# Optimization experiments

Hardware: AMD Instinct MI355X
Metric: run time of the kernel (lower is better)

## Reference

```python
import jax, jax.numpy as jnp
import numpy as np

VOCAB = 32000
MAX_LEN = 40
DIM_HIDDEN = 1024
DIM_WORD = 512
DIM_VID = 4096
BOS_ID = 0


def lstm_step(x, h, c, w_ih, w_hh, b_ih, b_hh):
    # torch LSTM gate order: i, f, g, o
    gates = x @ w_ih.T + b_ih + h @ w_hh.T + b_hh  # (1, 4H)
    i, f, g, o = jnp.split(gates, 4, axis=-1)
    c_new = jax.nn.sigmoid(f) * c + jax.nn.sigmoid(i) * jnp.tanh(g)
    h_new = jax.nn.sigmoid(o) * jnp.tanh(c_new)
    return h_new, c_new


def setup_inputs() -> dict:
    key = jax.random.key(0)
    ks = jax.random.split(key, 12)
    s1 = 1.0 / np.sqrt(DIM_HIDDEN)
    H = DIM_HIDDEN
    return {
        "vid_feats": jax.random.normal(ks[0], (1, DIM_VID), jnp.float32),
        "w_ih1": jax.random.uniform(ks[1], (4 * H, DIM_VID), jnp.float32, -s1, s1),
        "w_hh1": jax.random.uniform(ks[2], (4 * H, H), jnp.float32, -s1, s1),
        "b_ih1": jax.random.uniform(ks[3], (4 * H,), jnp.float32, -s1, s1),
        "b_hh1": jax.random.uniform(ks[4], (4 * H,), jnp.float32, -s1, s1),
        "w_ih2": jax.random.uniform(ks[5], (4 * H, H + DIM_WORD), jnp.float32, -s1, s1),
        "w_hh2": jax.random.uniform(ks[6], (4 * H, H), jnp.float32, -s1, s1),
        "b_ih2": jax.random.uniform(ks[7], (4 * H,), jnp.float32, -s1, s1),
        "b_hh2": jax.random.uniform(ks[8], (4 * H,), jnp.float32, -s1, s1),
        "emb": jax.random.normal(ks[9], (VOCAB, DIM_WORD), jnp.float32),
        "w_out": jax.random.uniform(ks[10], (VOCAB, H), jnp.float32, -s1, s1),
        "b_out": jax.random.uniform(ks[11], (VOCAB,), jnp.float32, -s1, s1),
    }


def reference(vid_feats, w_ih1, w_hh1, b_ih1, b_hh1, w_ih2, w_hh2, b_ih2, b_hh2, emb, w_out, b_out):
    H = DIM_HIDDEN
    zeros_h = jnp.zeros((1, H), vid_feats.dtype)
    pad_vid = jnp.zeros((1, DIM_VID), vid_feats.dtype)
    pad_word = jnp.zeros((1, DIM_WORD), vid_feats.dtype)

    # encode phase: one step of each LSTM (vid feats + padding word)
    h1, c1 = lstm_step(vid_feats, zeros_h, zeros_h, w_ih1, w_hh1, b_ih1, b_hh1)
    inp2 = jnp.concatenate([h1, pad_word], axis=1)
    h2, c2 = lstm_step(inp2, zeros_h, zeros_h, w_ih2, w_hh2, b_ih2, b_hh2)
    idx0 = jnp.int32(BOS_ID)  # output2 is overwritten with bos_id in the source

    def step(carry, _):
        h1, c1, h2, c2, idx = carry
        h1, c1 = lstm_step(pad_vid, h1, c1, w_ih1, w_hh1, b_ih1, b_hh1)
        embedded = emb[idx].reshape(1, -1)  # (1, dim_word)
        inp2 = jnp.concatenate([h1, embedded], axis=1)
        h2, c2 = lstm_step(inp2, h2, c2, w_ih2, w_hh2, b_ih2, b_hh2)
        logits = h2 @ w_out.T + b_out  # (1, vocab)
        logp = jax.nn.log_softmax(logits, axis=-1)
        # faithful to source: topk over the HIDDEN output, not logits
        idx = jnp.argmax(h2[0]).astype(jnp.int32)
        return (h1, c1, h2, c2, idx), logp

    _, prob_sentence = jax.lax.scan(step, (h1, c1, h2, c2, idx0), None, length=MAX_LEN - 1)
    return prob_sentence  # (max_len-1, 1, vocab)
```

## Files before the change

### kernel.cpp

```cpp
#include <hip/hip_runtime.h>
#include <hip/hip_fp16.h>

typedef unsigned u32x4 __attribute__((ext_vector_type(4)));

#define HID    1024
#define DVID   4096
#define DWORD  512
#define XLEN   (HID + DWORD)
#define NVOCAB 32000
#define NSTEP  39
#define NT     256
#define NWPB   (NT / 64)
#define TT     8
#define NPASS  ((NSTEP + TT - 1) / TT)
#define NEG_BIG (-3.402823466e38f)
#define MAGIC_VAL 0x5EEDF11Du

#define CTRL_BYTES 65536
#define RBAR_W   0
#define H2F_W    1024
#define FBAR_W   2048
#define G1_OFF   65536
#define G2A_OFF  (G1_OFF  + 32768)
#define G2B_OFF  (G2A_OFF + 32768)
#define H2B_OFF  (G2B_OFF + 32768)
#define PM_OFF   (H2B_OFF + 159744)
#define PS_OFF   (PM_OFF  + 159744)
#define MAGIC_OFF (PS_OFF + 159744)
#define W16_OFF  (MAGIC_OFF + 256)
#define W16_BYTES ((size_t)NVOCAB * HID * 2)
#define WIH2_OFF (W16_OFF + W16_BYTES)
#define WIH2_BYTES ((size_t)DVID * XLEN * 2)
#define WHH1_OFF (WIH2_OFF + WIH2_BYTES)
#define WHH_BYTES ((size_t)DVID * HID * 2)
#define WHH2_OFF (WHH1_OFF + WHH_BYTES)
#define WS_T1 ((size_t)W16_OFF + W16_BYTES)
#define WS_T2 ((size_t)WHH2_OFF + WHH_BYTES)

#define FENCE_REL() __builtin_amdgcn_fence(__ATOMIC_RELEASE, "agent")
#define FENCE_ACQ() __builtin_amdgcn_fence(__ATOMIC_ACQUIRE, "agent")

__device__ __forceinline__ float gload(float* p) {
    return __hip_atomic_load(p, __ATOMIC_RELAXED, __HIP_MEMORY_SCOPE_AGENT);
}
__device__ __forceinline__ void gstore(float* p, float v) {
    __hip_atomic_store(p, v, __ATOMIC_RELAXED, __HIP_MEMORY_SCOPE_AGENT);
}
__device__ __forceinline__ unsigned gloadu(unsigned* p) {
    return __hip_atomic_load(p, __ATOMIC_RELAXED, __HIP_MEMORY_SCOPE_AGENT);
}
__device__ __forceinline__ void gstoreu(unsigned* p, unsigned v) {
    __hip_atomic_store(p, v, __ATOMIC_RELAXED, __HIP_MEMORY_SCOPE_AGENT);
}

__device__ __forceinline__ float fast_sigmoid(float x) { return 1.f / (1.f + __expf(-x)); }
__device__ __forceinline__ float fast_tanh(float x)    { return 1.f - 2.f / (__expf(2.f * x) + 1.f); }

__device__ __forceinline__ float wave_reduce(float v) {
#pragma unroll
    for (int o = 32; o; o >>= 1) v += __shfl_xor(v, o, 64);
    return v;
}
__device__ __forceinline__ int wave_reduce_i(int v) {
// ... 11 lines not shown
    if (v > m) { s = s * __expf(m - v) + 1.f; m = v; } else s += __expf(v - m);
}

template<int LEN>
__device__ __forceinline__ float row_dotT(const float* __restrict__ w, const float* x, int lane) {
    float a = 0.f;
#pragma unroll
    for (int q = lane * 4; q < LEN; q += 256) {
        float4 wv = *(const float4*)(w + q);
        float4 xv = *(const float4*)(x + q);
        a = fmaf(wv.x, xv.x, a); a = fmaf(wv.y, xv.y, a);
        a = fmaf(wv.z, xv.z, a); a = fmaf(wv.w, xv.w, a);
    }
    return wave_reduce(a);
}
__device__ __forceinline__ void row_dot2(const float* __restrict__ wa, const float* xa,
                                         const float* __restrict__ wb, const float* xb,
                                         int lane, float& ra, float& rb) {
    float a = 0.f, b = 0.f;
#pragma unroll
    for (int q = lane * 4; q < HID; q += 256) {
        float4 w1 = *(const float4*)(wa + q);
        float4 w2 = *(const float4*)(wb + q);
        float4 x1 = *(const float4*)(xa + q);
        float4 x2 = *(const float4*)(xb + q);
        a = fmaf(w1.x, x1.x, a); a = fmaf(w1.y, x1.y, a);
        a = fmaf(w1.z, x1.z, a); a = fmaf(w1.w, x1.w, a);
        b = fmaf(w2.x, x2.x, b); b = fmaf(w2.y, x2.y, b);
        b = fmaf(w2.z, x2.z, b); b = fmaf(w2.w, x2.w, b);
    }
    ra = wave_reduce(a); rb = wave_reduce(b);
}

__device__ __forceinline__ float hlo(unsigned u) {
    return __half2float(__ushort_as_half((unsigned short)(u & 0xffffu)));
}
__device__ __forceinline__ float hhi(unsigned u) {
    return __half2float(__ushort_as_half((unsigned short)(u >> 16)));
}
__device__ __forceinline__ u32x4 ntld(const unsigned short* p) {
    return __builtin_nontemporal_load((const u32x4*)p);
}

template<int LEN>
__device__ __forceinline__ float row_dotT_h(const unsigned short* __restrict__ w, const float* x, int lane) {
    float a = 0.f;
#pragma unroll
    for (int q = lane * 8; q < LEN; q += 512) {
        u32x4 u = *(const u32x4*)(w + q);
        float4 x0 = *(const float4*)(x + q);
        float4 x1 = *(const float4*)(x + q + 4);
        a = fmaf(hlo(u.x), x0.x, a); a = fmaf(hhi(u.x), x0.y, a);
        a = fmaf(hlo(u.y), x0.z, a); a = fmaf(hhi(u.y), x0.w, a);
        a = fmaf(hlo(u.z), x1.x, a); a = fmaf(hhi(u.z), x1.y, a);
        a = fmaf(hlo(u.w), x1.z, a); a = fmaf(hhi(u.w), x1.w, a);
    }
    return wave_reduce(a);
}
__device__ __forceinline__ void row_dot2_h(const unsigned short* __restrict__ wa, const float* xa,
                                           const unsigned short* __restrict__ wb, const float* xb,
                                           int lane, float& ra, float& rb) {
    float a = 0.f, b = 0.f;
#pragma unroll
    for (int q = lane * 8; q < HID; q += 512) {
        u32x4 ua = *(const u32x4*)(wa + q);
        u32x4 ub = *(const u32x4*)(wb + q);
        float4 xa0 = *(const float4*)(xa + q);
        float4 xa1 = *(const float4*)(xa + q + 4);
        float4 xb0 = *(const float4*)(xb + q);
        float4 xb1 = *(const float4*)(xb + q + 4);
        a = fmaf(hlo(ua.x), xa0.x, a); a = fmaf(hhi(ua.x), xa0.y, a);
        a = fmaf(hlo(ua.y), xa0.z, a); a = fmaf(hhi(ua.y), xa0.w, a);
        a = fmaf(hlo(ua.z), xa1.x, a); a = fmaf(hhi(ua.z), xa1.y, a);
        a = fmaf(hlo(ua.w), xa1.z, a); a = fmaf(hhi(ua.w), xa1.w, a);
        b = fmaf(hlo(ub.x), xb0.x, b); b = fmaf(hhi(ub.x), xb0.y, b);
        b = fmaf(hlo(ub.y), xb0.z, b); b = fmaf(hhi(ub.y), xb0.w, b);
        b = fmaf(hlo(ub.z), xb1.x, b); b = fmaf(hhi(ub.z), xb1.y, b);
        b = fmaf(hlo(ub.w), xb1.z, b); b = fmaf(hhi(ub.w), xb1.w, b);
    }
    ra = wave_reduce(a); rb = wave_reduce(b);
}

#define DOT16H(acc, u0, u1)                                                \
    acc = fmaf(hlo(u0.x), x0.x, acc); acc = fmaf(hhi(u0.x), x0.y, acc);    \
    acc = fmaf(hlo(u0.y), x0.z, acc); acc = fmaf(hhi(u0.y), x0.w, acc);    \
    acc = fmaf(hlo(u0.z), x1.x, acc); acc = fmaf(hhi(u0.z), x1.y, acc);    \
    acc = fmaf(hlo(u0.w), x1.z, acc); acc = fmaf(hhi(u0.w), x1.w, acc);    \
    acc = fmaf(hlo(u1.x), x2.x, acc); acc = fmaf(hhi(u1.x), x2.y, acc);    \
    acc = fmaf(hlo(u1.y), x2.z, acc); acc = fmaf(hhi(u1.y), x2.w, acc);    \
    acc = fmaf(hlo(u1.z), x3.x, acc); acc = fmaf(hhi(u1.z), x3.y, acc);    \
    acc = fmaf(hlo(u1.w), x3.z, acc); acc = fmaf(hhi(u1.w), x3.w, acc);

__device__ __forceinline__ void lstm_update1(float* G, float* c, float* h, int tid) {
#pragma unroll
    for (int j = tid; j < HID; j += NT) {
        float gi = gload(G + j), gf = gload(G + j + HID);
        float gg = gload(G + j + 2 * HID), go = gload(G + j + 3 * HID);
        float cn = fast_sigmoid(gf) * c[j] + fast_sigmoid(gi) * fast_tanh(gg);
        c[j] = cn;
        h[j] = fast_sigmoid(go) * fast_tanh(cn);
    }
}
__device__ __forceinline__ void lstm_update2(float* Ga, float* Gb, float* c, float* h, int tid) {
#pragma unroll
    for (int j = tid; j < HID; j += NT) {
        float gi = gload(Ga + j) + gload(Gb + j);
        float gf = gload(Ga + j + HID) + gload(Gb + j + HID);
        float gg = gload(Ga + j + 2 * HID) + gload(Gb + j + 2 * HID);
        float go = gload(Ga + j + 3 * HID) + gload(Gb + j + 3 * HID);
        float cn = fast_sigmoid(gf) * c[j] + fast_sigmoid(gi) * fast_tanh(gg);
        c[j] = cn;
        h[j] = fast_sigmoid(go) * fast_tanh(cn);
    }
}

__device__ __forceinline__ void gbar(unsigned* base, int line, unsigned target, int tid, int lane) {
    __syncthreads();
    if (tid < 64) {
        if (lane == 0)
            __hip_atomic_fetch_add(base + line * 32, 1u, __ATOMIC_RELAXED, __HIP_MEMORY_SCOPE_AGENT);
        for (;;) {
            unsigned v = (lane < 16) ? gloadu(base + lane * 32) : 0u;
            if ((unsigned)wave_reduce_i((int)v) >= target) break;
            __builtin_amdgcn_s_sleep(4);
        }
    }
    __syncthreads();
}
// ... 18 lines not shown
        r.y = __half_as_ushort(__float2half(v.y));
        r.z = __half_as_ushort(__float2half(v.z));
        r.w = __half_as_ushort(__float2half(v.w));
        *(ushort4*)(d + off) = r;
    }
}

__global__ __launch_bounds__(NT, 4) void seq2seq_kernel(
    const float* __restrict__ vid,
    const float* __restrict__ w_ih1, const float* __restrict__ w_hh1,
    const float* __restrict__ b_ih1, const float* __restrict__ b_hh1,
    const float* __restrict__ w_ih2, const float* __restrict__ w_hh2,
    const float* __restrict__ b_ih2, const float* __restrict__ b_hh2,
    const float* __restrict__ emb,  const float* __restrict__ w_out,
    const float* __restrict__ b_out,
    int use16, int useh, int nr, int nl,
    float* __restrict__ out, char* wsb, unsigned* magicp)
{
    const int tid  = threadIdx.x;
    const int lane = tid & 63;
    const int wib  = tid >> 6;
    const int bid  = blockIdx.x;
    const int nb   = nr + nl;

    unsigned* ctrl = (unsigned*)wsb;
    unsigned* rbar = ctrl + RBAR_W;
    unsigned* h2f  = ctrl + H2F_W;
    unsigned* fbar = ctrl + FBAR_W;
    float* G1g = (float*)(wsb + G1_OFF);
    float* G2a = (float*)(wsb + G2A_OFF);
    float* G2b = (float*)(wsb + G2B_OFF);
    float* h2b = (float*)(wsb + H2B_OFF);
    float* PM  = (float*)(wsb + PM_OFF);
    float* PS  = (float*)(wsb + PS_OFF);
    const unsigned short* w16   = (const unsigned short*)(wsb + W16_OFF);
    const unsigned short* wih2h = (const unsigned short*)(wsb + WIH2_OFF);
    const unsigned short* whh1h = (const unsigned short*)(wsb + WHH1_OFF);
    const unsigned short* whh2h = (const unsigned short*)(wsb + WHH2_OFF);

    __shared__ __align__(16) float sMem[TT * HID];
    float* sX  = sMem;
    float* sC1 = sMem + XLEN;
    float* sC2 = sMem + XLEN + HID;
    float* sH2 = sMem + XLEN + 2 * HID;
    float* sXT = sMem;
    __shared__ float sRm[NWPB], sRs[NWPB];
    __shared__ int   sRi[NWPB];
    __shared__ int   sIdx;
    __shared__ float sPm[NWPB][TT], sPs[NWPB][TT];
    __shared__ float sOff[NSTEP];

    if (magicp && bid == 0 && tid == 0) gstoreu(magicp, MAGIC_VAL);

    const bool isrec = (bid < nr);
    const int  lb    = bid - nr;
    const int  chunk = (NVOCAB + nl - 1) / nl;
    const int  begin = isrec ? 0 : lb * chunk;
    const int  end   = isrec ? 0 : min(begin + chunk, NVOCAB);
    const bool active = (!isrec) && (begin < end);
    unsigned tgt = 0;

    for (int j = tid; j < HID; j += NT) { sC1[j] = 0.f; sC2[j] = 0.f; }
    if (tid == 0) sIdx = 0;
    __syncthreads();
    {
        const int nwr = nb * NWPB, gw = bid * NWPB + wib;
        {
            int ch = (4096 + nwr - 1) / nwr;
            int b0 = gw * ch, e0 = min(b0 + ch, 4096);
            for (int r = b0; r < e0; ++r) {
                float v = row_dotT<DVID>(w_ih1 + (size_t)r * DVID, vid, lane);
                if (lane == 0) gstore(&G1g[4096 + r], v + b_ih1[r] + b_hh1[r]);
            }
        }
        tgt += nb; gbar(rbar, bid & 15, tgt, tid, lane);
        lstm_update1(G1g + 4096, sC1, sX, tid);
        for (int j = tid; j < DWORD; j += NT) sX[HID + j] = 0.f;
        __syncthreads();
        {
            int ch = (8192 + nwr - 1) / nwr;
            int b0 = gw * ch, e0 = min(b0 + ch, 8192);
            for (int task = b0; task < e0; ++task) {
                if (task < 4096) {
                    int r = task;
                    float v = row_dotT<XLEN>(w_ih2 + (size_t)r * XLEN, sX, lane);
                    if (lane == 0) gstore(&G2a[4096 + r], v + b_ih2[r] + b_hh2[r]);
                } else {
                    int r = task - 4096;
                    float v = row_dotT<HID>(w_hh1 + (size_t)r * HID, sX, lane);
                    if (lane == 0) { gstore(&G1g[r], v + b_ih1[r] + b_hh1[r]); gstore(&G2b[4096 + r], 0.f); }
                }
            }
        }
        tgt += nb; gbar(rbar, bid & 15, tgt, tid, lane);
    }

    if (isrec) {
        __builtin_amdgcn_s_setprio(2);
        const int nwr = nr * NWPB, gw = bid * NWPB + wib;
        lstm_update2(G2a + 4096, G2b + 4096, sC2, sH2, tid);
        __syncthreads();

        for (int t = 0; t < NSTEP; ++t) {
            const int cb = (t & 1) * 4096, nb2 = ((t + 1) & 1) * 4096;
            lstm_update1(G1g + cb, sC1, sX, tid);
            {
                const float* erow = emb + (size_t)sIdx * DWORD;
                for (int j = tid; j < DWORD; j += NT) sX[HID + j] = erow[j];
            }
            __syncthreads();
            {
                int ch = (8192 + nwr - 1) / nwr;
                int b0 = gw * ch, e0 = min(b0 + ch, 8192);
                if (useh) {
                    for (int task = b0; task < e0; ++task) {
                        if (task < 4096) {
                            int r = task;
                            float v = row_dotT_h<XLEN>(wih2h + (size_t)r * XLEN, sX, lane);
                            if (lane == 0) gstore(&G2a[cb + r], v + b_ih2[r] + b_hh2[r]);
                        } else {
                            int r = task - 4096;
                            float va, vb;
                            row_dot2_h(whh2h + (size_t)r * HID, sH2,
                                       whh1h + (size_t)r * HID, sX, lane, va, vb);
                            if (lane == 0) {
                                gstore(&G2b[cb + r], va);
                                if (t < NSTEP - 1) gstore(&G1g[nb2 + r], vb + b_ih1[r] + b_hh1[r]);
                            }
                        }
                    }
                } else {
                    for (int task = b0; task < e0; ++task) {
                        if (task < 4096) {
                            int r = task;
                            float v = row_dotT<XLEN>(w_ih2 + (size_t)r * XLEN, sX, lane);
                            if (lane == 0) gstore(&G2a[cb + r], v + b_ih2[r] + b_hh2[r]);
                        } else {
                            int r = task - 4096;
                            float va, vb;
                            row_dot2(w_hh2 + (size_t)r * HID, sH2,
                                     w_hh1 + (size_t)r * HID, sX, lane, va, vb);
                            if (lane == 0) {
                                gstore(&G2b[cb + r], va);
                                if (t < NSTEP - 1) gstore(&G1g[nb2 + r], vb + b_ih1[r] + b_hh1[r]);
                            }
                        }
                    }
                }
            }
            tgt += nr; gbar(rbar, bid & 15, tgt, tid, lane);

            lstm_update2(G2a + cb, G2b + cb, sC2, sH2, tid);
            __syncthreads();
            if (bid == 0)
                for (int j = tid; j < HID; j += NT) gstore(&h2b[(size_t)t * HID + j], sH2[j]);
            {
                float bm = NEG_BIG; int bi = 0;
                for (int j = tid; j < HID; j += NT) {
                    float v = sH2[j];
                    if (v > bm) { bm = v; bi = j; }
                }
#pragma unroll
                for (int o = 32; o; o >>= 1) {
                    float vm = __shfl_xor(bm, o, 64); int vi = __shfl_xor(bi, o, 64);
                    if (vm > bm || (vm == bm && vi < bi)) { bm = vm; bi = vi; }
                }
                if (lane == 0) { sRm[wib] = bm; sRi[wib] = bi; }
                __syncthreads();
                if (tid == 0) {
                    float m0 = sRm[0]; int i0 = sRi[0];
                    for (int w = 1; w < NWPB; ++w)
                        if (sRm[w] > m0 || (sRm[w] == m0 && sRi[w] < i0)) { m0 = sRm[w]; i0 = sRi[w]; }
                    sIdx = i0;
                }
            }
            __syncthreads();
            if (bid == 0 && tid == 0) {
#pragma unroll
                for (int i = 0; i < 8; ++i)
                    gstoreu(h2f + i * 32, (unsigned)(t + 1));
            }
        }
    } else if (active) {
        unsigned* myflag = h2f + (lb & 7) * 32;

        if (use16) {
            unsigned acc = 0u;
            for (int r = begin + wib; r < end; r += NWPB) {
                u32x4 a = ntld(w16 + (size_t)r * HID + lane * 8);
                u32x4 b2 = ntld(w16 + (size_t)r * HID + 512 + lane * 8);
                acc += a.x + b2.x;
            }
            asm volatile("" :: "v"(acc));
        }

        for (int pass = 0; pass < NPASS; ++pass) {
            const int t0 = pass * TT;
            const int tn = (NSTEP - t0 < TT) ? (NSTEP - t0) : TT;
            const unsigned twait = (unsigned)(t0 + tn);
            if (tid == 0) {
                while (gloadu(myflag) < twait) __builtin_amdgcn_s_sleep(16);
            }
            __syncthreads();
            for (int i = tid; i < tn * HID; i += NT)
                sXT[i] = gload(&h2b[(size_t)t0 * HID + i]);
            __syncthreads();

            float m[TT], s[TT];
#pragma unroll
            for (int k = 0; k < TT; ++k) { m[k] = NEG_BIG; s[k] = 0.f; }

            if (use16) {
                const int qe = begin + ((end - begin) & ~3);
                for (int r = begin + wib * 4; r < qe; r += NWPB * 4) {
                    const unsigned short* wp = w16 + (size_t)r * HID + lane * 8;
                    u32x4 ua0 = ntld(wp);            u32x4 ua1 = ntld(wp + 512);
                    u32x4 ub0 = ntld(wp + HID);      u32x4 ub1 = ntld(wp + HID + 512);
                    u32x4 uc0 = ntld(wp + 2 * HID);  u32x4 uc1 = ntld(wp + 2 * HID + 512);
                    u32x4 ud0 = ntld(wp + 3 * HID);  u32x4 ud1 = ntld(wp + 3 * HID + 512);
                    float b0v = b_out[r], b1v = b_out[r + 1], b2v = b_out[r + 2], b3v = b_out[r + 3];
#pragma unroll
                    for (int k = 0; k < TT; ++k) {
                        if (t0 + k < NSTEP) {
                            const float* xp = sXT + k * HID + lane * 8;
                            float4 x0 = *(const float4*)(xp);
                            float4 x1 = *(const float4*)(xp + 4);
                            float4 x2 = *(const float4*)(xp + 512);
                            float4 x3 = *(const float4*)(xp + 516);
                            float a0 = 0.f, a1 = 0.f, a2 = 0.f, a3 = 0.f;
                            DOT16H(a0, ua0, ua1)
                            DOT16H(a1, ub0, ub1)
                            DOT16H(a2, uc0, uc1)
                            DOT16H(a3, ud0, ud1)
                            float v0 = wave_reduce(a0) + b0v;
                            float v1 = wave_reduce(a1) + b1v;
                            float v2 = wave_reduce(a2) + b2v;
                            float v3 = wave_reduce(a3) + b3v;
                            if (lane == 0) {
                                float* op = out + (size_t)(t0 + k) * NVOCAB + r;
                                op[0] = v0; op[1] = v1; op[2] = v2; op[3] = v3;
                            }
                            online_upd(m[k], s[k], v0); online_upd(m[k], s[k], v1);
                            online_upd(m[k], s[k], v2); online_upd(m[k], s[k], v3);
                        }
                    }
                }
                for (int r = qe + wib; r < end; r += NWPB) {
                    const unsigned short* wp = w16 + (size_t)r * HID + lane * 8;
                    u32x4 u0 = ntld(wp);
                    u32x4 u1 = ntld(wp + 512);
                    float bv = b_out[r];
#pragma unroll
                    for (int k = 0; k < TT; ++k) {
                        if (t0 + k < NSTEP) {
                            const float* xp = sXT + k * HID + lane * 8;
                            float4 x0 = *(const float4*)(xp);
                            float4 x1 = *(const float4*)(xp + 4);
                            float4 x2 = *(const float4*)(xp + 512);
                            float4 x3 = *(const float4*)(xp + 516);
                            float a = 0.f;
                            DOT16H(a, u0, u1)
                            float v = wave_reduce(a) + bv;
                            if (lane == 0) out[(size_t)(t0 + k) * NVOCAB + r] = v;
                            online_upd(m[k], s[k], v);
                        }
                    }
                }
            } else {
                for (int r = begin + wib; r < end; r += NWPB) {
                    const float* wp = w_out + (size_t)r * HID;
                    float bv = b_out[r];
#pragma unroll
                    for (int k = 0; k < TT; ++k) {
                        if (t0 + k < NSTEP) {
                            float v = row_dotT<HID>(wp, sXT + k * HID, lane) + bv;
                            if (lane == 0) out[(size_t)(t0 + k) * NVOCAB + r] = v;
                            online_upd(m[k], s[k], v);
                        }
                    }
                }
            }

            if (lane == 0) {
#pragma unroll
                for (int k = 0; k < TT; ++k) { sPm[wib][k] = m[k]; sPs[wib][k] = s[k]; }
            }
            __syncthreads();
            if (tid == 0) {
#pragma unroll
                for (int k = 0; k < TT; ++k) {
// ... 58 lines not shown
    const float* b_ih1 = (const float*)d_in[3];
    const float* b_hh1 = (const float*)d_in[4];
    const float* w_ih2 = (const float*)d_in[5];
    const float* w_hh2 = (const float*)d_in[6];
    const float* b_ih2 = (const float*)d_in[7];
    const float* b_hh2 = (const float*)d_in[8];
    const float* emb   = (const float*)d_in[9];
    const float* w_out = (const float*)d_in[10];
    const float* b_out = (const float*)d_in[11];
    float* out = (float*)d_out;
    char* wsb  = (char*)d_ws;

    int use16 = (ws_size >= WS_T1) ? 1 : 0;
    int useh  = (ws_size >= WS_T2) ? 1 : 0;
    unsigned* magicp = (ws_size >= (size_t)MAGIC_OFF + 256) ? (unsigned*)(wsb + MAGIC_OFF) : (unsigned*)0;

    hipMemsetAsync(d_ws, 0, CTRL_BYTES, stream);

    if (use16 && magicp) {
        int n0 = NVOCAB * HID;
        int n1 = useh ? DVID * XLEN : 0;
        int n2 = useh ? DVID * HID : 0;
        int n3 = useh ? DVID * HID : 0;
        cvt_all<<<dim3(2048), dim3(256), 0, stream>>>(
            w_out, w_ih2, w_hh1, w_hh2,
            (unsigned short*)(wsb + W16_OFF), (unsigned short*)(wsb + WIH2_OFF),
            (unsigned short*)(wsb + WHH1_OFF), (unsigned short*)(wsb + WHH2_OFF),
            n0, n1, n2, n3, magicp);
    } else {
        use16 = 0; useh = 0;
    }

    int occ = 0;
    if (hipOccupancyMaxActiveBlocksPerMultiprocessor(&occ, seq2seq_kernel, NT, 0) != hipSuccess || occ < 1)
        occ = 1;
    int nb = occ * 256;
    if (nb > 1024) nb = 1024;
    nb &= ~3;
    if (nb < 4) nb = 4;
    int nr = nb >> 2, nl = nb - nr;

    void* args[] = { &vid, &w_ih1, &w_hh1, &b_ih1, &b_hh1,
                     &w_ih2, &w_hh2, &b_ih2, &b_hh2,
                     &emb, &w_out, &b_out, &use16, &useh, &nr, &nl, &out, &wsb, &magicp };
    hipLaunchCooperativeKernel((const void*)seq2seq_kernel,
                               dim3(nb), dim3(NT), args, 0, stream);
}
```

Before: 1.665 ms.

## Partition LSTM recurrence into 64 unit-owning blocks with packed fp16 dot2 math

Restructures the recurrent phase so a fixed set of 64 blocks each own a slice of hidden units. Each block computes all four gates for its units locally and exchanges only h vectors through global buffers, instead of the whole gate vector being reduced and redistributed. It also switches the fp16 weight dot products to packed fdot2 with fp16-packed activations, and restructures the vocab projection to reuse each weight load across 8 time steps. The argmax is now done through per-block partials. This adds an extra grid barrier in the encode phase, changes the block split, and adds fp16 rounding of activations.

```diff
diff --git a/kernel.cpp b/kernel.cpp
--- a/kernel.cpp
+++ b/kernel.cpp
@@ -2,6 +2,8 @@
 #include <hip/hip_fp16.h>
 
 typedef unsigned u32x4 __attribute__((ext_vector_type(4)));
+typedef unsigned u32x2 __attribute__((ext_vector_type(2)));
+typedef _Float16 h2v  __attribute__((ext_vector_type(2)));
 
 #define HID    1024
 #define DVID   4096
@@ -11,42 +13,47 @@
 #define NSTEP  39
 #define NT     256
 #define NWPB   (NT / 64)
+#define NR     64
+#define U      (HID / NR)
 #define TT     8
 #define NPASS  ((NSTEP + TT - 1) / TT)
 #define NEG_BIG (-3.402823466e38f)
-#define MAGIC_VAL 0x5EEDF11Du
+#define MAGIC_VAL 0x5EEDF22Du
 
 #define CTRL_BYTES 65536
 #define RBAR_W   0
 #define H2F_W    1024
 #define FBAR_W   2048
-#define G1_OFF   65536
-#define G2A_OFF  (G1_OFF  + 32768)
-#define G2B_OFF  (G2A_OFF + 32768)
-#define H2B_OFF  (G2B_OFF + 32768)
-#define PM_OFF   (H2B_OFF + 159744)
-#define PS_OFF   (PM_OFF  + 159744)
-#define MAGIC_OFF (PS_OFF + 159744)
-#define W16_OFF  (MAGIC_OFF + 256)
-#define W16_BYTES ((size_t)NVOCAB * HID * 2)
-#define WIH2_OFF (W16_OFF + W16_BYTES)
+#define GE_OFF    65536
+#define GE2_OFF   (GE_OFF  + 16384)
+#define H1B_OFF   (GE2_OFF + 16384)
+#define H2BF_OFF  (H1B_OFF + 8192)
+#define PV_OFF    (H2BF_OFF + 8192)
+#define PI_OFF    (PV_OFF  + 512)
+#define H2B_OFF   (PI_OFF  + 512)
+#define PM_OFF    (H2B_OFF + 159744)
+#define PS_OFF    (PM_OFF  + 159744)
+#define MAGIC_OFF (PS_OFF  + 159744)
+#define W16_OFF   (MAGIC_OFF + 256)
+#define W16_BYTES  ((size_t)NVOCAB * HID * 2)
+#define WIH2_OFF  (W16_OFF + W16_BYTES)
 #define WIH2_BYTES ((size_t)DVID * XLEN * 2)
-#define WHH1_OFF (WIH2_OFF + WIH2_BYTES)
-#define WHH_BYTES ((size_t)DVID * HID * 2)
-#define WHH2_OFF (WHH1_OFF + WHH_BYTES)
-#define WS_T1 ((size_t)W16_OFF + W16_BYTES)
-#define WS_T2 ((size_t)WHH2_OFF + WHH_BYTES)
+#define WHH1_OFF  (WIH2_OFF + WIH2_BYTES)
+#define WHH_BYTES  ((size_t)DVID * HID * 2)
+#define WHH2_OFF  (WHH1_OFF + WHH_BYTES)
+#define WS_T1  ((size_t)W16_OFF + W16_BYTES)
+#define WS_T2  ((size_t)WHH2_OFF + WHH_BYTES)
 
 #define FENCE_REL() __builtin_amdgcn_fence(__ATOMIC_RELEASE, "agent")
 #define FENCE_ACQ() __builtin_amdgcn_fence(__ATOMIC_ACQUIRE, "agent")
 
-__device__ __forceinline__ float gload(float* p) {
-    return __hip_atomic_load(p, __ATOMIC_RELAXED, __HIP_MEMORY_SCOPE_AGENT);
+__device__ __forceinline__ float gload(const float* p) {
+    return __hip_atomic_load((const float*)p, __ATOMIC_RELAXED, __HIP_MEMORY_SCOPE_AGENT);
 }
 __device__ __forceinline__ void gstore(float* p, float v) {
     __hip_atomic_store(p, v, __ATOMIC_RELAXED, __HIP_MEMORY_SCOPE_AGENT);
 }
-__device__ __forceinline__ unsigned gloadu(unsigned* p) {
+__device__ __forceinline__ unsigned gloadu(const unsigned* p) {
     return __hip_atomic_load(p, __ATOMIC_RELAXED, __HIP_MEMORY_SCOPE_AGENT);
 }
 __device__ __forceinline__ void gstoreu(unsigned* p, unsigned v) {
@@ -88,104 +95,20 @@
     }
     return wave_reduce(a);
 }
-__device__ __forceinline__ void row_dot2(const float* __restrict__ wa, const float* xa,
-                                         const float* __restrict__ wb, const float* xb,
-                                         int lane, float& ra, float& rb) {
-    float a = 0.f, b = 0.f;
-#pragma unroll
-    for (int q = lane * 4; q < HID; q += 256) {
-        float4 w1 = *(const float4*)(wa + q);
-        float4 w2 = *(const float4*)(wb + q);
-        float4 x1 = *(const float4*)(xa + q);
-        float4 x2 = *(const float4*)(xb + q);
-        a = fmaf(w1.x, x1.x, a); a = fmaf(w1.y, x1.y, a);
-        a = fmaf(w1.z, x1.z, a); a = fmaf(w1.w, x1.w, a);
-        b = fmaf(w2.x, x2.x, b); b = fmaf(w2.y, x2.y, b);
-        b = fmaf(w2.z, x2.z, b); b = fmaf(w2.w, x2.w, b);
-    }
-    ra = wave_reduce(a); rb = wave_reduce(b);
-}
-
-__device__ __forceinline__ float hlo(unsigned u) {
-    return __half2float(__ushort_as_half((unsigned short)(u & 0xffffu)));
-}
-__device__ __forceinline__ float hhi(unsigned u) {
-    return __half2float(__ushort_as_half((unsigned short)(u >> 16)));
-}
-__device__ __forceinline__ u32x4 ntld(const unsigned short* p) {
+
+__device__ __forceinline__ float fd2(unsigned w, unsigned x, float a) {
+    return __builtin_amdgcn_fdot2(__builtin_bit_cast(h2v, w), __builtin_bit_cast(h2v, x), a, false);
+}
+__device__ __forceinline__ unsigned pk2(float a, float b) {
+    unsigned short lo = __half_as_ushort(__float2half(a));
+    unsigned short hi = __half_as_ushort(__float2half(b));
+    return (unsigned)lo | ((unsigned)hi << 16);
+}
+__device__ __forceinline__ u32x4 ntld4(const unsigned* p) {
     return __builtin_nontemporal_load((const u32x4*)p);
 }
-
-template<int LEN>
-__device__ __forceinline__ float row_dotT_h(const unsigned short* __restrict__ w, const float* x, int lane) {
-    float a = 0.f;
-#pragma unroll
-    for (int q = lane * 8; q < LEN; q += 512) {
-        u32x4 u = *(const u32x4*)(w + q);
-        float4 x0 = *(const float4*)(x + q);
-        float4 x1 = *(const float4*)(x + q + 4);
-        a = fmaf(hlo(u.x), x0.x, a); a = fmaf(hhi(u.x), x0.y, a);
-        a = fmaf(hlo(u.y), x0.z, a); a = fmaf(hhi(u.y), x0.w, a);
-        a = fmaf(hlo(u.z), x1.x, a); a = fmaf(hhi(u.z), x1.y, a);
-        a = fmaf(hlo(u.w), x1.z, a); a = fmaf(hhi(u.w), x1.w, a);
-    }
-    return wave_reduce(a);
-}
-__device__ __forceinline__ void row_dot2_h(const unsigned short* __restrict__ wa, const float* xa,
-                                           const unsigned short* __restrict__ wb, const float* xb,
-                                           int lane, float& ra, float& rb) {
-    float a = 0.f, b = 0.f;
-#pragma unroll
-    for (int q = lane * 8; q < HID; q += 512) {
-        u32x4 ua = *(const u32x4*)(wa + q);
-        u32x4 ub = *(const u32x4*)(wb + q);
-        float4 xa0 = *(const float4*)(xa + q);
-        float4 xa1 = *(const float4*)(xa + q + 4);
-        float4 xb0 = *(const float4*)(xb + q);
-        float4 xb1 = *(const float4*)(xb + q + 4);
-        a = fmaf(hlo(ua.x), xa0.x, a); a = fmaf(hhi(ua.x), xa0.y, a);
-        a = fmaf(hlo(ua.y), xa0.z, a); a = fmaf(hhi(ua.y), xa0.w, a);
-        a = fmaf(hlo(ua.z), xa1.x, a); a = fmaf(hhi(ua.z), xa1.y, a);
-        a = fmaf(hlo(ua.w), xa1.z, a); a = fmaf(hhi(ua.w), xa1.w, a);
-        b = fmaf(hlo(ub.x), xb0.x, b); b = fmaf(hhi(ub.x), xb0.y, b);
-        b = fmaf(hlo(ub.y), xb0.z, b); b = fmaf(hhi(ub.y), xb0.w, b);
-        b = fmaf(hlo(ub.z), xb1.x, b); b = fmaf(hhi(ub.z), xb1.y, b);
-        b = fmaf(hlo(ub.w), xb1.z, b); b = fmaf(hhi(ub.w), xb1.w, b);
-    }
-    ra = wave_reduce(a); rb = wave_reduce(b);
-}
-
-#define DOT16H(acc, u0, u1)                                                \
-    acc = fmaf(hlo(u0.x), x0.x, acc); acc = fmaf(hhi(u0.x), x0.y, acc);    \
-    acc = fmaf(hlo(u0.y), x0.z, acc); acc = fmaf(hhi(u0.y), x0.w, acc);    \
-    acc = fmaf(hlo(u0.z), x1.x, acc); acc = fmaf(hhi(u0.z), x1.y, acc);    \
-    acc = fmaf(hlo(u0.w), x1.z, acc); acc = fmaf(hhi(u0.w), x1.w, acc);    \
-    acc = fmaf(hlo(u1.x), x2.x, acc); acc = fmaf(hhi(u1.x), x2.y, acc);    \
-    acc = fmaf(hlo(u1.y), x2.z, acc); acc = fmaf(hhi(u1.y), x2.w, acc);    \
-    acc = fmaf(hlo(u1.z), x3.x, acc); acc = fmaf(hhi(u1.z), x3.y, acc);    \
-    acc = fmaf(hlo(u1.w), x3.z, acc); acc = fmaf(hhi(u1.w), x3.w, acc);
-
-__device__ __forceinline__ void lstm_update1(float* G, float* c, float* h, int tid) {
-#pragma unroll
-    for (int j = tid; j < HID; j += NT) {
-        float gi = gload(G + j), gf = gload(G + j + HID);
-        float gg = gload(G + j + 2 * HID), go = gload(G + j + 3 * HID);
-        float cn = fast_sigmoid(gf) * c[j] + fast_sigmoid(gi) * fast_tanh(gg);
-        c[j] = cn;
-        h[j] = fast_sigmoid(go) * fast_tanh(cn);
-    }
-}
-__device__ __forceinline__ void lstm_update2(float* Ga, float* Gb, float* c, float* h, int tid) {
-#pragma unroll
-    for (int j = tid; j < HID; j += NT) {
-        float gi = gload(Ga + j) + gload(Gb + j);
-        float gf = gload(Ga + j + HID) + gload(Gb + j + HID);
-        float gg = gload(Ga + j + 2 * HID) + gload(Gb + j + 2 * HID);
-        float go = gload(Ga + j + 3 * HID) + gload(Gb + j + 3 * HID);
-        float cn = fast_sigmoid(gf) * c[j] + fast_sigmoid(gi) * fast_tanh(gg);
-        c[j] = cn;
-        h[j] = fast_sigmoid(go) * fast_tanh(cn);
-    }
+__device__ __forceinline__ u32x2 ntld2(const unsigned* p) {
+    return __builtin_nontemporal_load((const u32x2*)p);
 }
 
 __device__ __forceinline__ void gbar(unsigned* base, int line, unsigned target, int tid, int lane) {
@@ -234,55 +157,49 @@
     const float* __restrict__ b_ih2, const float* __restrict__ b_hh2,
     const float* __restrict__ emb,  const float* __restrict__ w_out,
     const float* __restrict__ b_out,
-    int use16, int useh, int nr, int nl,
+    int use16, int useh, int nl,
     float* __restrict__ out, char* wsb, unsigned* magicp)
 {
     const int tid  = threadIdx.x;
     const int lane = tid & 63;
     const int wib  = tid >> 6;
     const int bid  = blockIdx.x;
-    const int nb   = nr + nl;
+    const int nb   = NR + nl;
 
     unsigned* ctrl = (unsigned*)wsb;
     unsigned* rbar = ctrl + RBAR_W;
     unsigned* h2f  = ctrl + H2F_W;
     unsigned* fbar = ctrl + FBAR_W;
-    float* G1g = (float*)(wsb + G1_OFF);
-    float* G2a = (float*)(wsb + G2A_OFF);
-    float* G2b = (float*)(wsb + G2B_OFF);
-    float* h2b = (float*)(wsb + H2B_OFF);
-    float* PM  = (float*)(wsb + PM_OFF);
-    float* PS  = (float*)(wsb + PS_OFF);
-    const unsigned short* w16   = (const unsigned short*)(wsb + W16_OFF);
-    const unsigned short* wih2h = (const unsigned short*)(wsb + WIH2_OFF);
-    const unsigned short* whh1h = (const unsigned short*)(wsb + WHH1_OFF);
-    const unsigned short* whh2h = (const unsigned short*)(wsb + WHH2_OFF);
-
-    __shared__ __align__(16) float sMem[TT * HID];
-    float* sX  = sMem;
-    float* sC1 = sMem + XLEN;
-    float* sC2 = sMem + XLEN + HID;
-    float* sH2 = sMem + XLEN + 2 * HID;
-    float* sXT = sMem;
-    __shared__ float sRm[NWPB], sRs[NWPB];
-    __shared__ int   sRi[NWPB];
-    __shared__ int   sIdx;
+    float* GE    = (float*)(wsb + GE_OFF);
+    float* GE2   = (float*)(wsb + GE2_OFF);
+    float* h1buf = (float*)(wsb + H1B_OFF);
+    float* h2buf = (float*)(wsb + H2BF_OFF);
+    float* PV    = (float*)(wsb + PV_OFF);
+    unsigned* PI = (unsigned*)(wsb + PI_OFF);
+    float* h2b   = (float*)(wsb + H2B_OFF);
+    float* PM    = (float*)(wsb + PM_OFF);
+    float* PS    = (float*)(wsb + PS_OFF);
+    const unsigned* w16u  = (const unsigned*)(wsb + W16_OFF);
+    const unsigned* wih2u = (const unsigned*)(wsb + WIH2_OFF);
+    const unsigned* whh1u = (const unsigned*)(wsb + WHH1_OFF);
+    const unsigned* whh2u = (const unsigned*)(wsb + WHH2_OFF);
+
+    __shared__ __align__(16) unsigned sBuf[4096];
+    __shared__ float sG2[64], sG1[64], sB2v[64], sB1v[64];
+    __shared__ float sC1a[U], sC2a[U], sHo[U];
     __shared__ float sPm[NWPB][TT], sPs[NWPB][TT];
     __shared__ float sOff[NSTEP];
 
     if (magicp && bid == 0 && tid == 0) gstoreu(magicp, MAGIC_VAL);
 
-    const bool isrec = (bid < nr);
-    const int  lb    = bid - nr;
+    const bool isrec = (bid < NR);
+    const int  lb    = bid - NR;
     const int  chunk = (NVOCAB + nl - 1) / nl;
     const int  begin = isrec ? 0 : lb * chunk;
     const int  end   = isrec ? 0 : min(begin + chunk, NVOCAB);
     const bool active = (!isrec) && (begin < end);
     unsigned tgt = 0;
 
-    for (int j = tid; j < HID; j += NT) { sC1[j] = 0.f; sC2[j] = 0.f; }
-    if (tid == 0) sIdx = 0;
-    __syncthreads();
     {
         const int nwr = nb * NWPB, gw = bid * NWPB + wib;
         {
@@ -290,12 +207,25 @@
             int b0 = gw * ch, e0 = min(b0 + ch, 4096);
             for (int r = b0; r < e0; ++r) {
                 float v = row_dotT<DVID>(w_ih1 + (size_t)r * DVID, vid, lane);
-                if (lane == 0) gstore(&G1g[4096 + r], v + b_ih1[r] + b_hh1[r]);
+                if (lane == 0) gstore(GE + r, v + b_ih1[r] + b_hh1[r]);
             }
         }
         tgt += nb; gbar(rbar, bid & 15, tgt, tid, lane);
-        lstm_update1(G1g + 4096, sC1, sX, tid);
-        for (int j = tid; j < DWORD; j += NT) sX[HID + j] = 0.f;
+        if (isrec && tid < U) {
+            int gu = bid * U + tid;
+            float gi = gload(GE + gu), gg = gload(GE + 2048 + gu), go = gload(GE + 3072 + gu);
+            float c1 = fast_sigmoid(gi) * fast_tanh(gg);
+            sC1a[tid] = c1;
+            gstore(h1buf + HID + gu, fast_sigmoid(go) * fast_tanh(c1));
+        }
+        tgt += nb; gbar(rbar, bid & 15, tgt, tid, lane);
+        float* sXf = (float*)sBuf;
+        for (int i = tid * 4; i < HID; i += NT * 4) {
+            float4 v;
+            v.x = gload(h1buf + HID + i);     v.y = gload(h1buf + HID + i + 1);
+            v.z = gload(h1buf + HID + i + 2); v.w = gload(h1buf + HID + i + 3);
+            *(float4*)(sXf + i) = v;
+        }
         __syncthreads();
         {
             int ch = (8192 + nwr - 1) / nwr;
@@ -303,12 +233,12 @@
             for (int task = b0; task < e0; ++task) {
                 if (task < 4096) {
                     int r = task;
-                    float v = row_dotT<XLEN>(w_ih2 + (size_t)r * XLEN, sX, lane);
-                    if (lane == 0) gstore(&G2a[4096 + r], v + b_ih2[r] + b_hh2[r]);
+                    float v = row_dotT<HID>(w_ih2 + (size_t)r * XLEN, sXf, lane);
+                    if (lane == 0) gstore(GE2 + r, v + b_ih2[r] + b_hh2[r]);
                 } else {
                     int r = task - 4096;
-                    float v = row_dotT<HID>(w_hh1 + (size_t)r * HID, sX, lane);
-                    if (lane == 0) { gstore(&G1g[r], v + b_ih1[r] + b_hh1[r]); gstore(&G2b[4096 + r], 0.f); }
+                    float v = row_dotT<HID>(w_hh1 + (size_t)r * HID, sXf, lane);
+                    if (lane == 0) gstore(GE + r, v + b_ih1[r] + b_hh1[r]);
                 }
             }
         }
@@ -317,98 +247,199 @@
 
     if (isrec) {
         __builtin_amdgcn_s_setprio(2);
-        const int nwr = nr * NWPB, gw = bid * NWPB + wib;
-        lstm_update2(G2a + 4096, G2b + 4096, sC2, sH2, tid);
-        __syncthreads();
+        if (tid < U) {
+            int gu = bid * U + tid;
+            float gi = gload(GE2 + gu), gg = gload(GE2 + 2048 + gu), go = gload(GE2 + 3072 + gu);
+            float c2 = fast_sigmoid(gi) * fast_tanh(gg);
+            sC2a[tid] = c2;
+            gstore(h2buf + HID + gu, fast_sigmoid(go) * fast_tanh(c2));
+            gi = gload(GE + gu); float gf = gload(GE + 1024 + gu);
+            gg = gload(GE + 2048 + gu); go = gload(GE + 3072 + gu);
+            float c1 = fast_sigmoid(gf) * sC1a[tid] + fast_sigmoid(gi) * fast_tanh(gg);
+            sC1a[tid] = c1;
+            gstore(h1buf + gu, fast_sigmoid(go) * fast_tanh(c1));
+        }
+        if (tid < 64) {
+            int rr = (tid & 3) * HID + bid * U + (tid >> 2);
+            sB2v[tid] = b_ih2[rr] + b_hh2[rr];
+            sB1v[tid] = b_ih1[rr] + b_hh1[rr];
+        }
+        tgt += NR; gbar(rbar, bid & 15, tgt, tid, lane);
+
+        unsigned* sXh  = sBuf;
+        unsigned* sH2h = sBuf + 768;
+        float*    sXf32 = (float*)sBuf;
+
+        const int g  = lane >> 2, gl = lane & 3;
+        const int d  = wib * 16 + g;
+        const int r2 = (d & 3) * HID + bid * U + (d >> 2);
 
         for (int t = 0; t < NSTEP; ++t) {
-            const int cb = (t & 1) * 4096, nb2 = ((t + 1) & 1) * 4096;
-            lstm_update1(G1g + cb, sC1, sX, tid);
-            {
-                const float* erow = emb + (size_t)sIdx * DWORD;
-                for (int j = tid; j < DWORD; j += NT) sX[HID + j] = erow[j];
+            if (wib == 0) {
+                unsigned idx = 0;
+                if (t > 0) {
+                    const int par = (t + 1) & 1;
+                    float av = gload(PV + par * NR + lane);
+                    unsigned ai = gloadu(PI + par * NR + lane);
+#pragma unroll
+                    for (int o = 32; o; o >>= 1) {
+                        float vm = __shfl_xor(av, o, 64);
+                        unsigned im = (unsigned)__shfl_xor((int)ai, o, 64);
+                        if (vm > av || (vm == av && im < ai)) { av = vm; ai = im; }
+                    }
+                    idx = ai;
+                }
+                const float* er = emb + (size_t)idx * DWORD + lane * 8;
+                float4 e0 = *(const float4*)(er), e1 = *(const float4*)(er + 4);
+                if (useh) {
+                    u32x4 p;
+                    p.x = pk2(e0.x, e0.y); p.y = pk2(e0.z, e0.w);
+                    p.z = pk2(e1.x, e1.y); p.w = pk2(e1.z, e1.w);
+                    *(u32x4*)(sXh + 512 + lane * 4) = p;
+                } else {
+                    *(float4*)(sXf32 + HID + lane * 8) = e0;
+                    *(float4*)(sXf32 + HID + lane * 8 + 4) = e1;
+                }
+            } else if (wib < 3) {
+                int j = tid - 64;
+                const float* hp = h1buf + (t & 1) * HID + j * 8;
+                float v[8];
+#pragma unroll
+                for (int e2 = 0; e2 < 8; ++e2) v[e2] = gload(hp + e2);
+                if (useh) {
+                    u32x4 p;
+                    p.x = pk2(v[0], v[1]); p.y = pk2(v[2], v[3]);
+                    p.z = pk2(v[4], v[5]); p.w = pk2(v[6], v[7]);
+                    *(u32x4*)(sXh + j * 4) = p;
+                } else {
+                    float4 a = {v[0], v[1], v[2], v[3]}, b = {v[4], v[5], v[6], v[7]};
+                    *(float4*)(sXf32 + j * 8) = a;
+                    *(float4*)(sXf32 + j * 8 + 4) = b;
+                }
+            } else {
+                int j = tid - 192;
+                const float* hp = h2buf + ((t + 1) & 1) * HID + j * 16;
+                float v[16];
+#pragma unroll
+                for (int e2 = 0; e2 < 16; ++e2) v[e2] = gload(hp + e2);
+                if (useh) {
+                    u32x4 p0, p1;
+                    p0.x = pk2(v[0], v[1]);  p0.y = pk2(v[2], v[3]);
+                    p0.z = pk2(v[4], v[5]);  p0.w = pk2(v[6], v[7]);
+                    p1.x = pk2(v[8], v[9]);  p1.y = pk2(v[10], v[11]);
+                    p1.z = pk2(v[12], v[13]); p1.w = pk2(v[14], v[15]);
+                    *(u32x4*)(sH2h + j * 8) = p0;
+                    *(u32x4*)(sH2h + j * 8 + 4) = p1;
+                } else {
+                    *(float4*)(sXf32 + 1536 + j * 16)      = {v[0], v[1], v[2], v[3]};
+                    *(float4*)(sXf32 + 1536 + j * 16 + 4)  = {v[4], v[5], v[6], v[7]};
+                    *(float4*)(sXf32 + 1536 + j * 16 + 8)  = {v[8], v[9], v[10], v[11]};
+                    *(float4*)(sXf32 + 1536 + j * 16 + 12) = {v[12], v[13], v[14], v[15]};
+                }
             }
             __syncthreads();
-            {
-                int ch = (8192 + nwr - 1) / nwr;
-                int b0 = gw * ch, e0 = min(b0 + ch, 8192);
-                if (useh) {
-                    for (int task = b0; task < e0; ++task) {
-                        if (task < 4096) {
-                            int r = task;
-                            float v = row_dotT_h<XLEN>(wih2h + (size_t)r * XLEN, sX, lane);
-                            if (lane == 0) gstore(&G2a[cb + r], v + b_ih2[r] + b_hh2[r]);
-                        } else {
-                            int r = task - 4096;
-                            float va, vb;
-                            row_dot2_h(whh2h + (size_t)r * HID, sH2,
-                                       whh1h + (size_t)r * HID, sX, lane, va, vb);
-                            if (lane == 0) {
-                                gstore(&G2b[cb + r], va);
-                                if (t < NSTEP - 1) gstore(&G1g[nb2 + r], vb + b_ih1[r] + b_hh1[r]);
-                            }
-                        }
-                    }
-                } else {
-                    for (int task = b0; task < e0; ++task) {
-                        if (task < 4096) {
-                            int r = task;
-                            float v = row_dotT<XLEN>(w_ih2 + (size_t)r * XLEN, sX, lane);
-                            if (lane == 0) gstore(&G2a[cb + r], v + b_ih2[r] + b_hh2[r]);
-                        } else {
-                            int r = task - 4096;
-                            float va, vb;
-                            row_dot2(w_hh2 + (size_t)r * HID, sH2,
-                                     w_hh1 + (size_t)r * HID, sX, lane, va, vb);
-                            if (lane == 0) {
-                                gstore(&G2b[cb + r], va);
-                                if (t < NSTEP - 1) gstore(&G1g[nb2 + r], vb + b_ih1[r] + b_hh1[r]);
-                            }
-                        }
-                    }
-                }
-            }
-            tgt += nr; gbar(rbar, bid & 15, tgt, tid, lane);
-
-            lstm_update2(G2a + cb, G2b + cb, sC2, sH2, tid);
+
+            float a2 = 0.f, a1 = 0.f;
+            if (useh) {
+                const unsigned* wr = wih2u + (size_t)r2 * 768;
+#pragma unroll
+                for (int j = 0; j < 48; ++j) {
+                    u32x4 w = *(const u32x4*)(wr + gl * 4 + j * 16);
+                    u32x4 x = *(const u32x4*)(sXh + gl * 4 + j * 16);
+                    a2 = fd2(w.x, x.x, a2); a2 = fd2(w.y, x.y, a2);
+                    a2 = fd2(w.z, x.z, a2); a2 = fd2(w.w, x.w, a2);
+                }
+                const unsigned* wr2 = whh2u + (size_t)r2 * 512;
+#pragma unroll
+                for (int j = 0; j < 32; ++j) {
+                    u32x4 w = *(const u32x4*)(wr2 + gl * 4 + j * 16);
+                    u32x4 x = *(const u32x4*)(sH2h + gl * 4 + j * 16);
+                    a2 = fd2(w.x, x.x, a2); a2 = fd2(w.y, x.y, a2);
+                    a2 = fd2(w.z, x.z, a2); a2 = fd2(w.w, x.w, a2);
+                }
+                if (t < NSTEP - 1) {
+                    const unsigned* wr1 = whh1u + (size_t)r2 * 512;
+#pragma unroll
+                    for (int j = 0; j < 32; ++j) {
+                        u32x4 w = *(const u32x4*)(wr1 + gl * 4 + j * 16);
+                        u32x4 x = *(const u32x4*)(sXh + gl * 4 + j * 16);
+                        a1 = fd2(w.x, x.x, a1); a1 = fd2(w.y, x.y, a1);
+                        a1 = fd2(w.z, x.z, a1); a1 = fd2(w.w, x.w, a1);
+                    }
+                }
+            } else {
+                const float* wr = w_ih2 + (size_t)r2 * XLEN;
+#pragma unroll 8
+                for (int j = 0; j < 96; ++j) {
+                    float4 w = *(const float4*)(wr + gl * 4 + j * 16);
+                    float4 x = *(const float4*)(sXf32 + gl * 4 + j * 16);
+                    a2 = fmaf(w.x, x.x, a2); a2 = fmaf(w.y, x.y, a2);
+                    a2 = fmaf(w.z, x.z, a2); a2 = fmaf(w.w, x.w, a2);
+                }
+                const float* wr2 = w_hh2 + (size_t)r2 * HID;
+#pragma unroll 8
+                for (int j = 0; j < 64; ++j) {
+                    float4 w = *(const float4*)(wr2 + gl * 4 + j * 16);
+                    float4 x = *(const float4*)(sXf32 + 1536 + gl * 4 + j * 16);
+                    a2 = fmaf(w.x, x.x, a2); a2 = fmaf(w.y, x.y, a2);
+                    a2 = fmaf(w.z, x.z, a2); a2 = fmaf(w.w, x.w, a2);
+                }
+                if (t < NSTEP - 1) {
+                    const float* wr1 = w_hh1 + (size_t)r2 * HID;
+#pragma unroll 8
+                    for (int j = 0; j < 64; ++j) {
+                        float4 w = *(const float4*)(wr1 + gl * 4 + j * 16);
+                        float4 x = *(const float4*)(sXf32 + gl * 4 + j * 16);
+                        a1 = fmaf(w.x, x.x, a1); a1 = fmaf(w.y, x.y, a1);
+                        a1 = fmaf(w.z, x.z, a1); a1 = fmaf(w.w, x.w, a1);
+                    }
+                }
+            }
+            a2 += __shfl_xor(a2, 1, 64); a2 += __shfl_xor(a2, 2, 64);
+            a1 += __shfl_xor(a1, 1, 64); a1 += __shfl_xor(a1, 2, 64);
+            if (gl == 0) { sG2[d] = a2 + sB2v[d]; sG1[d] = a1 + sB1v[d]; }
             __syncthreads();
-            if (bid == 0)
-                for (int j = tid; j < HID; j += NT) gstore(&h2b[(size_t)t * HID + j], sH2[j]);
-            {
-                float bm = NEG_BIG; int bi = 0;
-                for (int j = tid; j < HID; j += NT) {
-                    float v = sH2[j];
-                    if (v > bm) { bm = v; bi = j; }
-                }
-#pragma unroll
-                for (int o = 32; o; o >>= 1) {
-                    float vm = __shfl_xor(bm, o, 64); int vi = __shfl_xor(bi, o, 64);
-                    if (vm > bm || (vm == bm && vi < bi)) { bm = vm; bi = vi; }
-                }
-                if (lane == 0) { sRm[wib] = bm; sRi[wib] = bi; }
-                __syncthreads();
-                if (tid == 0) {
-                    float m0 = sRm[0]; int i0 = sRi[0];
-                    for (int w = 1; w < NWPB; ++w)
-                        if (sRm[w] > m0 || (sRm[w] == m0 && sRi[w] < i0)) { m0 = sRm[w]; i0 = sRi[w]; }
-                    sIdx = i0;
+
+            if (tid < U) {
+                int gu = bid * U + tid;
+                float gi = sG2[tid * 4], gf = sG2[tid * 4 + 1];
+                float gg = sG2[tid * 4 + 2], go = sG2[tid * 4 + 3];
+                float c2 = fast_sigmoid(gf) * sC2a[tid] + fast_sigmoid(gi) * fast_tanh(gg);
+                sC2a[tid] = c2;
+                float hv = fast_sigmoid(go) * fast_tanh(c2);
+                gstore(h2buf + (t & 1) * HID + gu, hv);
+                gstore(h2b + (size_t)t * HID + gu, hv);
+                sHo[tid] = hv;
+                if (t < NSTEP - 1) {
+                    gi = sG1[tid * 4]; gf = sG1[tid * 4 + 1];
+                    gg = sG1[tid * 4 + 2]; go = sG1[tid * 4 + 3];
+                    float c1 = fast_sigmoid(gf) * sC1a[tid] + fast_sigmoid(gi) * fast_tanh(gg);
+                    sC1a[tid] = c1;
+                    gstore(h1buf + ((t + 1) & 1) * HID + gu, fast_sigmoid(go) * fast_tanh(c1));
                 }
             }
             __syncthreads();
+            if (tid == 0) {
+                float bm = sHo[0]; int bi = 0;
+                for (int uu = 1; uu < U; ++uu) if (sHo[uu] > bm) { bm = sHo[uu]; bi = uu; }
+                gstore(PV + (t & 1) * NR + bid, bm);
+                gstoreu(PI + (t & 1) * NR + bid, (unsigned)(bid * U + bi));
+            }
+            tgt += NR; gbar(rbar, bid & 15, tgt, tid, lane);
             if (bid == 0 && tid == 0) {
 #pragma unroll
-                for (int i = 0; i < 8; ++i)
-                    gstoreu(h2f + i * 32, (unsigned)(t + 1));
+                for (int i = 0; i < 8; ++i) gstoreu(h2f + i * 32, (unsigned)(t + 1));
             }
         }
     } else if (active) {
         unsigned* myflag = h2f + (lb & 7) * 32;
+        unsigned* sXT2 = sBuf;
 
         if (use16) {
             unsigned acc = 0u;
             for (int r = begin + wib; r < end; r += NWPB) {
-                u32x4 a = ntld(w16 + (size_t)r * HID + lane * 8);
-                u32x4 b2 = ntld(w16 + (size_t)r * HID + 512 + lane * 8);
+                u32x4 a = ntld4(w16u + (size_t)r * 512 + lane * 8);
+                u32x4 b2 = ntld4(w16u + (size_t)r * 512 + lane * 8 + 4);
                 acc += a.x + b2.x;
             }
             asm volatile("" :: "v"(acc));
@@ -417,13 +448,15 @@
         for (int pass = 0; pass < NPASS; ++pass) {
             const int t0 = pass * TT;
             const int tn = (NSTEP - t0 < TT) ? (NSTEP - t0) : TT;
-            const unsigned twait = (unsigned)(t0 + tn);
             if (tid == 0) {
-                while (gloadu(myflag) < twait) __builtin_amdgcn_s_sleep(16);
+                while (gloadu(myflag) < (unsigned)(t0 + tn)) __builtin_amdgcn_s_sleep(32);
             }
             __syncthreads();
-            for (int i = tid; i < tn * HID; i += NT)
-                sXT[i] = gload(&h2b[(size_t)t0 * HID + i]);
+            for (int wdx = tid; wdx < tn * 512; wdx += NT) {
+                float f0 = gload(h2b + (size_t)t0 * HID + wdx * 2);
+                float f1 = gload(h2b + (size_t)t0 * HID + wdx * 2 + 1);
+                sXT2[wdx] = pk2(f0, f1);
+            }
             __syncthreads();
 
             float m[TT], s[TT];
@@ -431,56 +464,61 @@
             for (int k = 0; k < TT; ++k) { m[k] = NEG_BIG; s[k] = 0.f; }
 
             if (use16) {
-                const int qe = begin + ((end - begin) & ~3);
-                for (int r = begin + wib * 4; r < qe; r += NWPB * 4) {
-                    const unsigned short* wp = w16 + (size_t)r * HID + lane * 8;
-                    u32x4 ua0 = ntld(wp);            u32x4 ua1 = ntld(wp + 512);
-                    u32x4 ub0 = ntld(wp + HID);      u32x4 ub1 = ntld(wp + HID + 512);
-                    u32x4 uc0 = ntld(wp + 2 * HID);  u32x4 uc1 = ntld(wp + 2 * HID + 512);
-                    u32x4 ud0 = ntld(wp + 3 * HID);  u32x4 ud1 = ntld(wp + 3 * HID + 512);
-                    float b0v = b_out[r], b1v = b_out[r + 1], b2v = b_out[r + 2], b3v = b_out[r + 3];
+                int r = begin + wib * 4;
+                for (; r + 3 < end; r += NWPB * 4) {
+                    float acc[4][TT];
+#pragma unroll
+                    for (int j = 0; j < 4; ++j)
+#pragma unroll
+                        for (int k = 0; k < TT; ++k) acc[j][k] = 0.f;
+#pragma unroll
+                    for (int it = 0; it < 4; ++it) {
+                        const int ci = it * 128 + lane * 2;
+                        u32x2 w0 = ntld2(w16u + (size_t)r * 512 + ci);
+                        u32x2 w1 = ntld2(w16u + (size_t)(r + 1) * 512 + ci);
+                        u32x2 w2 = ntld2(w16u + (size_t)(r + 2) * 512 + ci);
+                        u32x2 w3 = ntld2(w16u + (size_t)(r + 3) * 512 + ci);
+#pragma unroll
+                        for (int k = 0; k < TT; ++k) {
+                            u32x2 x = *(const u32x2*)(sXT2 + k * 512 + ci);
+                            acc[0][k] = fd2(w0.x, x.x, acc[0][k]); acc[0][k] = fd2(w0.y, x.y, acc[0][k]);
+                            acc[1][k] = fd2(w1.x, x.x, acc[1][k]); acc[1][k] = fd2(w1.y, x.y, acc[1][k]);
+                            acc[2][k] = fd2(w2.x, x.x, acc[2][k]); acc[2][k] = fd2(w2.y, x.y, acc[2][k]);
+                            acc[3][k] = fd2(w3.x, x.x, acc[3][k]); acc[3][k] = fd2(w3.y, x.y, acc[3][k]);
+                        }
+                    }
+#pragma unroll
+                    for (int j = 0; j < 4; ++j) {
+                        float bv = b_out[r + j];
+#pragma unroll
+                        for (int k = 0; k < TT; ++k) {
+                            if (t0 + k < NSTEP) {
+                                float v = wave_reduce(acc[j][k]) + bv;
+                                if (lane == 0) out[(size_t)(t0 + k) * NVOCAB + r + j] = v;
+                                online_upd(m[k], s[k], v);
+                            }
+                        }
+                    }
+                }
+                for (; r < end; ++r) {
+                    float a1v[TT];
+#pragma unroll
+                    for (int k = 0; k < TT; ++k) a1v[k] = 0.f;
+#pragma unroll
+                    for (int it = 0; it < 4; ++it) {
+                        const int ci = it * 128 + lane * 2;
+                        u32x2 w0 = ntld2(w16u + (size_t)r * 512 + ci);
+#pragma unroll
+                        for (int k = 0; k < TT; ++k) {
+                            u32x2 x = *(const u32x2*)(sXT2 + k * 512 + ci);
+                            a1v[k] = fd2(w0.x, x.x, a1v[k]); a1v[k] = fd2(w0.y, x.y, a1v[k]);
+                        }
+                    }
+                    float bv = b_out[r];
 #pragma unroll
                     for (int k = 0; k < TT; ++k) {
                         if (t0 + k < NSTEP) {
-                            const float* xp = sXT + k * HID + lane * 8;
-                            float4 x0 = *(const float4*)(xp);
-                            float4 x1 = *(const float4*)(xp + 4);
-                            float4 x2 = *(const float4*)(xp + 512);
-                            float4 x3 = *(const float4*)(xp + 516);
-                            float a0 = 0.f, a1 = 0.f, a2 = 0.f, a3 = 0.f;
-                            DOT16H(a0, ua0, ua1)
-                            DOT16H(a1, ub0, ub1)
-                            DOT16H(a2, uc0, uc1)
-                            DOT16H(a3, ud0, ud1)
-                            float v0 = wave_reduce(a0) + b0v;
-                            float v1 = wave_reduce(a1) + b1v;
-                            float v2 = wave_reduce(a2) + b2v;
-                            float v3 = wave_reduce(a3) + b3v;
-                            if (lane == 0) {
-                                float* op = out + (size_t)(t0 + k) * NVOCAB + r;
-                                op[0] = v0; op[1] = v1; op[2] = v2; op[3] = v3;
-                            }
-                            online_upd(m[k], s[k], v0); online_upd(m[k], s[k], v1);
-                            online_upd(m[k], s[k], v2); online_upd(m[k], s[k], v3);
-                        }
-                    }
-                }
-                for (int r = qe + wib; r < end; r += NWPB) {
-                    const unsigned short* wp = w16 + (size_t)r * HID + lane * 8;
-                    u32x4 u0 = ntld(wp);
-                    u32x4 u1 = ntld(wp + 512);
-                    float bv = b_out[r];
-#pragma unroll
-                    for (int k = 0; k < TT; ++k) {
-                        if (t0 + k < NSTEP) {
-                            const float* xp = sXT + k * HID + lane * 8;
-                            float4 x0 = *(const float4*)(xp);
-                            float4 x1 = *(const float4*)(xp + 4);
-                            float4 x2 = *(const float4*)(xp + 512);
-                            float4 x3 = *(const float4*)(xp + 516);
-                            float a = 0.f;
-                            DOT16H(a, u0, u1)
-                            float v = wave_reduce(a) + bv;
+                            float v = wave_reduce(a1v[k]) + bv;
                             if (lane == 0) out[(size_t)(t0 + k) * NVOCAB + r] = v;
                             online_upd(m[k], s[k], v);
                         }
@@ -488,12 +526,18 @@
                 }
             } else {
                 for (int r = begin + wib; r < end; r += NWPB) {
-                    const float* wp = w_out + (size_t)r * HID;
                     float bv = b_out[r];
-#pragma unroll
                     for (int k = 0; k < TT; ++k) {
                         if (t0 + k < NSTEP) {
-                            float v = row_dotT<HID>(wp, sXT + k * HID, lane) + bv;
+                            float a = 0.f;
+                            for (int qq = lane * 4; qq < HID; qq += 256) {
+                                float4 w = *(const float4*)(w_out + (size_t)r * HID + qq);
+                                a = fmaf(w.x, gload(h2b + (size_t)(t0 + k) * HID + qq), a);
+                                a = fmaf(w.y, gload(h2b + (size_t)(t0 + k) * HID + qq + 1), a);
+                                a = fmaf(w.z, gload(h2b + (size_t)(t0 + k) * HID + qq + 2), a);
+                                a = fmaf(w.w, gload(h2b + (size_t)(t0 + k) * HID + qq + 3), a);
+                            }
+                            float v = wave_reduce(a) + bv;
                             if (lane == 0) out[(size_t)(t0 + k) * NVOCAB + r] = v;
                             online_upd(m[k], s[k], v);
                         }
@@ -582,10 +626,11 @@
     int use16 = (ws_size >= WS_T1) ? 1 : 0;
     int useh  = (ws_size >= WS_T2) ? 1 : 0;
     unsigned* magicp = (ws_size >= (size_t)MAGIC_OFF + 256) ? (unsigned*)(wsb + MAGIC_OFF) : (unsigned*)0;
+    if (!magicp) { use16 = 0; useh = 0; }
 
     hipMemsetAsync(d_ws, 0, CTRL_BYTES, stream);
 
-    if (use16 && magicp) {
+    if (use16) {
         int n0 = NVOCAB * HID;
         int n1 = useh ? DVID * XLEN : 0;
         int n2 = useh ? DVID * HID : 0;
@@ -595,8 +640,6 @@
             (unsigned short*)(wsb + W16_OFF), (unsigned short*)(wsb + WIH2_OFF),
             (unsigned short*)(wsb + WHH1_OFF), (unsigned short*)(wsb + WHH2_OFF),
             n0, n1, n2, n3, magicp);
-    } else {
-        use16 = 0; useh = 0;
     }
 
     int occ = 0;
@@ -604,13 +647,12 @@
         occ = 1;
     int nb = occ * 256;
     if (nb > 1024) nb = 1024;
-    nb &= ~3;
-    if (nb < 4) nb = 4;
-    int nr = nb >> 2, nl = nb - nr;
+    if (nb < 128) nb = 128;
+    int nl = nb - NR;
 
     void* args[] = { &vid, &w_ih1, &w_hh1, &b_ih1, &b_hh1,
                      &w_ih2, &w_hh2, &b_ih2, &b_hh2,
-                     &emb, &w_out, &b_out, &use16, &useh, &nr, &nl, &out, &wsb, &magicp };
+                     &emb, &w_out, &b_out, &use16, &useh, &nl, &out, &wsb, &magicp };
     hipLaunchCooperativeKernel((const void*)seq2seq_kernel,
                                dim3(nb), dim3(NT), args, 0, stream);
 }
```

New measurement: 3.140 ms. 88.5% more time.
